# Performance work log

Measured on AMD Instinct MI355X. Metric: run time of the kernel, lower is better.

Reference implementation:

```python
import jax, jax.numpy as jnp
import numpy as np

HID = 2048
NEXP = 16
BRD = max(64, HID // 8)        # block_router_dim = 256
BATCH, SEQ = 4, 8192
BASE_BS, MAX_BS = 512, 2048
BASE_THR, BASE_BUDGET = 0.6, 0.3


def _adjust(seq_len):
    # mirrors _adjust_parameters_for_length (static: depends only on shape)
    if seq_len <= 4096:
        return BASE_BS, BASE_THR, BASE_BUDGET
    elif seq_len <= 16384:
        return min(1024, MAX_BS), BASE_THR * 1.1, BASE_BUDGET * 0.7
    else:
        scale = min(seq_len / 16384, 4)
        return min(int(BASE_BS * scale), MAX_BS), BASE_THR * 1.2, BASE_BUDGET * (1.0 / scale)


def _layernorm(x, g, b, eps=1e-5):
    m = x.mean(-1, keepdims=True)
    v = ((x - m) ** 2).mean(-1, keepdims=True)
    return (x - m) / jnp.sqrt(v + eps) * g + b


def setup_inputs() -> dict:
    key = jax.random.key(0)
    k = jax.random.split(key, 6)
    return {
        "hidden_states": jax.random.normal(k[0], (BATCH, SEQ, HID), jnp.float32),
        # block_router: Linear(H->256) -> LN -> GELU -> Linear(256->E)
        "bw1": jax.random.normal(k[1], (HID, BRD), jnp.float32) * 0.02,
        "bb1": jnp.zeros((BRD,), jnp.float32),
        "ln_g": jnp.ones((BRD,), jnp.float32),
        "ln_b": jnp.zeros((BRD,), jnp.float32),
        # final block-router layer scaled up so block entropies spread around the
        # 0.66 threshold and both routing branches are exercised
        "bw2": jax.random.normal(k[2], (BRD, NEXP), jnp.float32) * 0.6,
        "bb2": jnp.zeros((NEXP,), jnp.float32),
        # token_router: Linear(H->H/2) -> GELU -> (Dropout: eval/identity) -> Linear(H/2->E)
        "tw1": jax.random.normal(k[3], (HID, HID // 2), jnp.float32) * 0.02,
        "tb1": jnp.zeros((HID // 2,), jnp.float32),
        "tw2": jax.random.normal(k[4], (HID // 2, NEXP), jnp.float32) * 0.02,
        "tb2": jnp.zeros((NEXP,), jnp.float32),
    }


def reference(hidden_states, bw1, bb1, ln_g, ln_b, bw2, bb2, tw1, tb1, tw2, tb2):
    B, S, H = hidden_states.shape
    E = bw2.shape[1]
    bs, thr, budget = _adjust(S)
    assert S % bs == 0, "reference assumes seq_len divisible by block_size"
    N = S // bs
    max_tok = int(S * budget)               # python int (static)
    k_budget = max(1, max_tok // bs)        # blocks_within_budget (static)

    # --- block-level routing ---
    block_repr = hidden_states.reshape(B, N, bs, H).mean(2)          # [B,N,H]
    h = _layernorm(block_repr @ bw1 + bb1, ln_g, ln_b)
    block_logits = jax.nn.gelu(h, approximate=False) @ bw2 + bb2     # [B,N,E]
    block_probs = jax.nn.softmax(block_logits, -1)
    p = block_probs + 1e-10
    entropy = -jnp.sum(p * jnp.log(p), -1) / jnp.log(jnp.float32(E))  # [B,N]

    mask1 = entropy > thr
    total_high = mask1.sum()
    # budget-based threshold adjustment (k-th largest high entropy)
    flat_ent = jnp.where(mask1.ravel(), entropy.ravel(), -jnp.inf)
    kth = jnp.sort(flat_ent)[::-1][k_budget - 1]
    cond = (total_high * bs > max_tok) & (total_high > 0) & (k_budget < total_high)
    mask2 = jnp.where(cond, entropy > kth, mask1)

    # sequential token budget over flattened (batch, block) row-major order
    cum = jnp.cumsum(mask2.ravel().astype(jnp.int32) * bs).reshape(B, N)
    token_flag = mask2 & (cum <= max_tok)            # per-token routing
    block_flag = (~mask1) | (mask2 & ~token_flag)    # block-level routing

    # block weight scatter: argmax one-hot * max prob (detached, torch uses .item())
    bw = jax.lax.stop_gradient(
        jax.nn.one_hot(jnp.argmax(block_probs, -1), E, dtype=block_probs.dtype)
        * jnp.max(block_probs, -1, keepdims=True))   # [B,N,E]

    # token-level routing computed densely, masked (dropout in eval mode = identity)
    th = jax.nn.gelu(hidden_states @ tw1 + tb1, approximate=False)
    token_probs = jax.nn.softmax(th @ tw2 + tb2, -1)  # [B,S,E]

    tf = jnp.repeat(token_flag, bs, axis=1)[..., None]   # [B,S,1]
    bf = jnp.repeat(block_flag, bs, axis=1)[..., None]
    bw_tok = jnp.repeat(bw, bs, axis=1)                  # [B,S,E]
    routing = jnp.where(tf, token_probs, jnp.where(bf, bw_tok, jnp.zeros((), hidden_states.dtype)))

    usage = routing.mean((0, 1))
    target = 1.0 / E
    aux = jnp.sum(target * jnp.log(target / (usage + 1e-10)))
    return routing, aux
```

## Files before the change

kernel.cpp:

```cpp
#include <hip/hip_runtime.h>
#include <math.h>

#define BB 4
#define SS 8192
#define HH 2048
#define EE 16
#define BRD_ 256
#define BSZ 1024
#define NN 8
#define NB 32
#define MAXTOK 1720
#define HHALF 1024
#define TC 16
#define ROWS 64
#define KSP 32
#define KL 64
#define JL 64

__device__ inline void wave_flags(const double* __restrict__ ent, int l,
                                  int& flag_out, int& fb_out) {
  const double THR = 0.6 * 1.1;
  double e = (l < NB) ? ent[l] : -INFINITY;
  bool m1 = (l < NB) && (e > THR);
  unsigned long long m1mask = __ballot(m1);
  int th = __popcll(m1mask);
  double sel = m1 ? e : -INFINITY;
  #pragma unroll
  for (int o = 32; o; o >>= 1) sel = fmax(sel, __shfl_xor(sel, o));
  bool m2 = (th >= 2) ? ((l < NB) && (e > sel)) : m1;
  unsigned long long m2mask = __ballot(m2);
  int cum = __popcll(m2mask & ((2ULL << l) - 1ULL)) * BSZ;
  bool tf = m2 && (cum <= MAXTOK);
  bool bf = (l < NB) && ((!m1) || (m2 && !tf));
  flag_out = tf ? 1 : (bf ? 2 : 0);
  unsigned long long tfmask = __ballot(tf);
  fb_out = tfmask ? (__ffsll(tfmask) - 1) : -1;
}

__global__ __launch_bounds__(256) void k_bmean(const float* __restrict__ x,
                                               double* __restrict__ part) {
  int wg = blockIdx.x;
  int bn = wg >> 4, tc = wg & 15;
  int b = bn >> 3, n = bn & 7;
  int tid = threadIdx.x;
  const float* base = x + ((size_t)(b * SS + n * BSZ + tc * ROWS) * HH);
  double a0=0,a1=0,a2=0,a3=0,a4=0,a5=0,a6=0,a7=0;
  #pragma unroll 4
  for (int t = 0; t < ROWS; ++t) {
    const float4* r = (const float4*)(base + (size_t)t * HH);
    float4 u = r[tid];
    float4 v = r[tid + 256];
    a0 += u.x; a1 += u.y; a2 += u.z; a3 += u.w;
    a4 += v.x; a5 += v.y; a6 += v.z; a7 += v.w;
  }
  double* p = part + ((size_t)bn * TC + tc) * HH;
  int hA = tid * 4, hB = 1024 + tid * 4;
  p[hA] = a0; p[hA+1] = a1; p[hA+2] = a2; p[hA+3] = a3;
  p[hB] = a4; p[hB+1] = a5; p[hB+2] = a6; p[hB+3] = a7;
}

__global__ __launch_bounds__(256) void k_g1(const double* __restrict__ part,
    const float* __restrict__ bw1, double* __restrict__ g1part) {
  __shared__ double brs[NB][KL];
  __shared__ float  wsm[KL][JL];
  int bid = blockIdx.x;
  int kq = bid >> 2, jt = bid & 3;
  int k0 = kq * KL, j0 = jt * JL;
  int tid = threadIdx.x;
  #pragma unroll
  for (int i = 0; i < 8; ++i) {
    int e = i * 256 + tid;
    int bn = e >> 6, k = e & 63;
    const double* pp = part + ((size_t)bn * TC) * HH + k0 + k;
    double s = 0;
    #pragma unroll
    for (int tc = 0; tc < TC; ++tc) s += pp[(size_t)tc * HH];
    brs[bn][k] = s * (1.0 / BSZ);
  }
  #pragma unroll
  for (int i = 0; i < 4; ++i) {
    int f = i * 256 + tid;
    int r = f >> 4, c4 = f & 15;
    float4 v = *(const float4*)(bw1 + (size_t)(k0 + r) * BRD_ + j0 + c4 * 4);
    *(float4*)&wsm[r][c4 * 4] = v;
  }
  __syncthreads();
  int j = tid & 63;
  int bh = (tid >> 6) * 8;
  double acc[8];
  #pragma unroll
  for (int r = 0; r < 8; ++r) acc[r] = 0;
  #pragma unroll 8
  for (int k = 0; k < KL; ++k) {
    double wv = (double)wsm[k][j];
    #pragma unroll
    for (int r = 0; r < 8; ++r) acc[r] += brs[bh + r][k] * wv;
  }
  #pragma unroll
  for (int r = 0; r < 8; ++r)
    g1part[((size_t)kq * NB + bh + r) * BRD_ + j0 + j] = acc[r];
}

__global__ __launch_bounds__(256) void k_router2(const double* __restrict__ g1part,
    const float* __restrict__ bb1, const float* __restrict__ lng, const float* __restrict__ lnb,
    const float* __restrict__ bw2, const float* __restrict__ bb2,
    double* __restrict__ ent, float* __restrict__ bwv, int* __restrict__ bwi) {
  __shared__ double tg[BRD_];
  __shared__ double p3[16][EE];
  __shared__ double red[4];
  __shared__ double l2[EE];
  __shared__ double bcast;
  int bn = blockIdx.x, tid = threadIdx.x;

  double a = (double)bb1[tid];
  #pragma unroll
  for (int kq = 0; kq < KSP; ++kq) a += g1part[((size_t)kq * NB + bn) * BRD_ + tid];

  double v = a;
  for (int o = 32; o; o >>= 1) v += __shfl_down(v, o);
  if ((tid & 63) == 0) red[tid >> 6] = v;
  __syncthreads();
  if (tid == 0) bcast = (red[0] + red[1] + red[2] + red[3]) * (1.0 / BRD_);
  __syncthreads();
  double m = bcast;
  double d = a - m;
  v = d * d;
  for (int o = 32; o; o >>= 1) v += __shfl_down(v, o);
  if ((tid & 63) == 0) red[tid >> 6] = v;
  __syncthreads();
  if (tid == 0) bcast = (red[0] + red[1] + red[2] + red[3]) * (1.0 / BRD_);
  __syncthreads();
  double var = bcast;
  double xn = d / sqrt(var + 1e-5) * (double)lng[tid] + (double)lnb[tid];
  tg[tid] = 0.5 * xn * (1.0 + erf(xn * 0.7071067811865476));
  __syncthreads();

  {
    int e = tid & 15, jc = tid >> 4;
    double s = 0;
    const float* w2 = bw2 + (size_t)(jc * 16) * EE + e;
    #pragma unroll
    for (int jj = 0; jj < 16; ++jj) s += tg[jc * 16 + jj] * (double)w2[jj * EE];
    p3[jc][e] = s;
  }
  __syncthreads();
  if (tid < EE) {
    double acc = (double)bb2[tid];
    #pragma unroll
    for (int jc = 0; jc < 16; ++jc) acc += p3[jc][tid];
    l2[tid] = acc;
  }
  __syncthreads();

  if (tid < 64) {
    int e = tid & 15;
    double le = l2[e];
    double mx = le;
    #pragma unroll
    for (int o = 1; o < 16; o <<= 1) mx = fmax(mx, __shfl_xor(mx, o));
    double pe = exp(le - mx);
    double se = pe;
    #pragma unroll
    for (int o = 1; o < 16; o <<= 1) se += __shfl_xor(se, o);
    double pr = pe / se;
    double q = pr + 1e-10;
    double term = -q * log(q);
    double es = term;
    #pragma unroll
    for (int o = 1; o < 16; o <<= 1) es += __shfl_xor(es, o);
    double mp = pr;
    #pragma unroll
    for (int o = 1; o < 16; o <<= 1) mp = fmax(mp, __shfl_xor(mp, o));
    unsigned long long eqm = __ballot((tid < 16) && (pr == mp));
    if (tid == 0) {
      ent[bn] = es / log(16.0);
      bwv[bn] = (float)mp;
      bwi[bn] = __ffsll(eqm) - 1;
    }
  }
}

__global__ __launch_bounds__(256) void k_out(const double* __restrict__ ent,
    const float* __restrict__ bwv, const int* __restrict__ bwi,
    const float* __restrict__ x, const float* __restrict__ tw1, const float* __restrict__ tb1,
    const float* __restrict__ tw2, float* __restrict__ routing, float* __restrict__ lpart) {
  __shared__ int flg_s[NB + 1];
  __shared__ float xs[64][33];
  __shared__ float wsm[32][65];
  __shared__ float ths[64][65];
  int tid = threadIdx.x;
  int bid = blockIdx.x;
  if (tid < 64) {
    int f, fb;
    wave_flags(ent, tid, f, fb);
    if (tid < NB) flg_s[tid] = f;
    if (tid == 0) flg_s[NB] = fb;
  }
  __syncthreads();

  if (bid < 256) {
    int bn = bid >> 3, seg = bid & 7;
    int fl = flg_s[bn];
    if (fl == 1) return;
    int b = bn >> 3, n = bn & 7;
    float4 z = make_float4(0.f, 0.f, 0.f, 0.f);
    float4 val = z;
    int c_hit = -1;
    if (fl == 2) {
      int ai = bwi[bn];
      c_hit = ai >> 2;
      ((float*)&val)[ai & 3] = bwv[bn];
    }
    float4* out = (float4*)(routing + ((size_t)(b * SS + n * BSZ + seg * 128) * EE));
    #pragma unroll
    for (int l = 0; l < 2; ++l) {
      int idx = l * 256 + tid;
      int c = idx & 3;
      out[idx] = (c == c_hit) ? val : z;
    }
    return;
  }

  int fb = flg_s[NB];
  if (fb < 0) return;
  int b = fb >> 3, n = fb & 7;
  int tb = bid - 256;
  int tg = tb >> 4, nc = tb & 15;
  int t0 = tg * 64, j0 = nc * 64;
  const float* xb = x + ((size_t)(b * SS + n * BSZ + t0) * HH);
  int tr = tid >> 4, tc = tid & 15;
  float acc[4][4];
  for (int i = 0; i < 4; ++i)
    for (int j = 0; j < 4; ++j) acc[i][j] = tb1[j0 + tc + j * 16];
  for (int k0 = 0; k0 < HH; k0 += 32) {
    #pragma unroll
    for (int l = 0; l < 8; ++l) {
      int idx = l * 256 + tid; int r = idx >> 5, c = idx & 31;
      xs[r][c] = xb[(size_t)r * HH + k0 + c];
    }
    #pragma unroll
    for (int l = 0; l < 8; ++l) {
      int idx = l * 256 + tid; int r = idx >> 6, c = idx & 63;
      wsm[r][c] = tw1[(size_t)(k0 + r) * HHALF + j0 + c];
    }
    __syncthreads();
    #pragma unroll
    for (int kk = 0; kk < 32; ++kk) {
      float xv[4], wv[4];
      for (int i = 0; i < 4; ++i) xv[i] = xs[tr + i * 16][kk];
      for (int j = 0; j < 4; ++j) wv[j] = wsm[kk][tc + j * 16];
      for (int i = 0; i < 4; ++i)
        for (int j = 0; j < 4; ++j) acc[i][j] += xv[i] * wv[j];
    }
    __syncthreads();
  }
  for (int i = 0; i < 4; ++i)
    for (int j = 0; j < 4; ++j) {
      float aa = acc[i][j];
      ths[tr + i * 16][tc + j * 16] = 0.5f * aa * (1.0f + erff(aa * 0.70710678f));
    }
  __syncthreads();
  float* lp = lpart + (size_t)nc * (BSZ * EE);
  #pragma unroll
  for (int l = 0; l < 4; ++l) {
    int idx = l * 256 + tid; int t = idx >> 4, e = idx & 15;
    float s = 0;
    #pragma unroll
    for (int jj = 0; jj < 64; ++jj) s += ths[t][jj] * tw2[(size_t)(j0 + jj) * EE + e];
    lp[(t0 + t) * EE + e] = s;
  }
}

__global__ __launch_bounds__(64) void k_toksoft(const double* __restrict__ ent,
    const float* __restrict__ lpart, const float* __restrict__ tb2,
    float* __restrict__ routing, double* __restrict__ upart) {
  int tid = threadIdx.x;
  int f_unused, fb;
  wave_flags(ent, tid, f_unused, fb);
  if (fb < 0) return;
  int b = fb >> 3, n = fb & 7;
  int w = blockIdx.x;
  int t = w * 64 + tid;
  float l[EE];
  #pragma unroll
  for (int e = 0; e < EE; ++e) {
    float s = tb2[e];
    #pragma unroll
    for (int nc = 0; nc < 16; ++nc) s += lpart[(size_t)nc * (BSZ * EE) + t * EE + e];
    l[e] = s;
  }
  float mx = l[0];
  for (int e = 1; e < EE; ++e) mx = fmaxf(mx, l[e]);
  float se = 0;
  for (int e = 0; e < EE; ++e) { l[e] = expf(l[e] - mx); se += l[e]; }
  float inv = 1.0f / se;
  for (int e = 0; e < EE; ++e) l[e] *= inv;
  float4* orow = (float4*)(routing + ((size_t)(b * SS + n * BSZ + t) * EE));
  orow[0] = make_float4(l[0], l[1], l[2], l[3]);
  orow[1] = make_float4(l[4], l[5], l[6], l[7]);
  orow[2] = make_float4(l[8], l[9], l[10], l[11]);
  orow[3] = make_float4(l[12], l[13], l[14], l[15]);
  for (int e = 0; e < EE; ++e) {
    double v = (double)l[e];
    for (int o = 32; o; o >>= 1) v += __shfl_down(v, o);
    if (tid == 0) upart[w * EE + e] = v;
  }
}

__global__ __launch_bounds__(256) void k_aux(const double* __restrict__ ent,
    const double* __restrict__ upart, const float* __restrict__ bwv,
    const int* __restrict__ bwi, float* __restrict__ outaux) {
  __shared__ int flg_s[NB + 1];
  __shared__ double up[16][EE];
  __shared__ double blkc[NB];
  __shared__ int    blke[NB];
  __shared__ double us[EE];
  int tid = threadIdx.x;
  if (tid < 64) {
    int f, fb;
    wave_flags(ent, tid, f, fb);
    if (tid < NB) flg_s[tid] = f;
    if (tid == 0) flg_s[NB] = fb;
  }
  __syncthreads();
  int fb = flg_s[NB];
  if (fb >= 0) up[tid >> 4][tid & 15] = upart[tid];
  if (tid < NB) {
    int f = flg_s[tid];
    blkc[tid] = (f == 2) ? (double)BSZ * (double)bwv[tid] : 0.0;
    blke[tid] = (f == 2) ? bwi[tid] : -1;
  }
  __syncthreads();
  if (tid < EE) {
    double s = 0;
    if (fb >= 0) for (int w = 0; w < 16; ++w) s += up[w][tid];
    for (int i = 0; i < NB; ++i) if (blke[i] == tid) s += blkc[i];
    us[tid] = s;
  }
  __syncthreads();
  if (tid == 0) {
    double aux = 0;
    const double target = 1.0 / EE;
    for (int e = 0; e < EE; ++e) {
      double u = us[e] / (double)(BB * SS);
      aux += target * log(target / (u + 1e-10));
    }
    *outaux = (float)aux;
  }
}

extern "C" void kernel_launch(void* const* d_in, const int* in_sizes, int n_in,
                              void* d_out, int out_size, void* d_ws, size_t ws_size,
                              hipStream_t stream) {
  const float* x   = (const float*)d_in[0];
  const float* bw1 = (const float*)d_in[1];
  const float* bb1 = (const float*)d_in[2];
  const float* lng = (const float*)d_in[3];
  const float* lnb = (const float*)d_in[4];
  const float* bw2 = (const float*)d_in[5];
  const float* bb2 = (const float*)d_in[6];
  const float* tw1 = (const float*)d_in[7];
  const float* tb1 = (const float*)d_in[8];
  const float* tw2 = (const float*)d_in[9];
  const float* tb2 = (const float*)d_in[10];
  float* routing = (float*)d_out;
  float* outaux = routing + (size_t)BB * SS * EE;

  char* w = (char*)d_ws;
  size_t off = 0;
  double* part  = (double*)(w + off); off += (size_t)NB * TC * HH * 8;
  double* g1p   = (double*)(w + off); off += (size_t)KSP * NB * BRD_ * 8;
  float*  lpart = (float*) (w + off); off += 16 * (size_t)BSZ * EE * 4;
  double* upart = (double*)(w + off); off += 16 * EE * 8;
  double* ent   = (double*)(w + off); off += NB * 8;
  float*  bwv   = (float*) (w + off); off += 256;
  int*    bwi   = (int*)   (w + off); off += 256;

  hipLaunchKernelGGL(k_bmean,   dim3(NB * TC), dim3(256), 0, stream, x, part);
  hipLaunchKernelGGL(k_g1,      dim3(128),     dim3(256), 0, stream, part, bw1, g1p);
  hipLaunchKernelGGL(k_router2, dim3(NB),      dim3(256), 0, stream, g1p,
                     bb1, lng, lnb, bw2, bb2, ent, bwv, bwi);
  hipLaunchKernelGGL(k_out,     dim3(512),     dim3(256), 0, stream, ent, bwv, bwi,
                     x, tw1, tb1, tw2, routing, lpart);
  hipLaunchKernelGGL(k_toksoft, dim3(16),      dim3(64),  0, stream, ent, lpart, tb2,
                     routing, upart);
  hipLaunchKernelGGL(k_aux,     dim3(1),       dim3(256), 0, stream, ent, upart, bwv, bwi, outaux);
}
```

Baseline: 74.51 us.

## Use bf16 MFMA for token router GEMM and fuse softmax with aux kernel

Replaces the scalar FP32 outer-product loop in the token-router first layer with bf16 MFMA 16x16x32 instructions. Inputs and weights are converted to bf16 while staged into LDS, and the weight tile is stored transposed. The token softmax and aux-loss kernels are merged into one 1024-thread block, which removes a launch and the upart workspace round trip. Rounding to bf16 lowers the precision of the hidden activations, which may push outputs past tolerance.

```diff
diff --git a/kernel.cpp b/kernel.cpp
--- a/kernel.cpp
+++ b/kernel.cpp
@@ -17,6 +17,15 @@
 #define KL 64
 #define JL 64
 
+typedef __attribute__((ext_vector_type(8))) short bf16x8;
+typedef __attribute__((ext_vector_type(4))) float f32x4;
+
+__device__ inline short f2bf(float f) {
+  unsigned u = __builtin_bit_cast(unsigned, f);
+  u += 0x7FFFu + ((u >> 16) & 1u);
+  return (short)(u >> 16);
+}
+
 __device__ inline void wave_flags(const double* __restrict__ ent, int l,
                                   int& flag_out, int& fb_out) {
   const double THR = 0.6 * 1.1;
@@ -185,8 +194,8 @@
     const float* __restrict__ x, const float* __restrict__ tw1, const float* __restrict__ tb1,
     const float* __restrict__ tw2, float* __restrict__ routing, float* __restrict__ lpart) {
   __shared__ int flg_s[NB + 1];
-  __shared__ float xs[64][33];
-  __shared__ float wsm[32][65];
+  __shared__ short xs_bf[64][72];
+  __shared__ short wsT[64][72];
   __shared__ float ths[64][65];
   int tid = threadIdx.x;
   int bid = blockIdx.x;
@@ -228,37 +237,50 @@
   int tg = tb >> 4, nc = tb & 15;
   int t0 = tg * 64, j0 = nc * 64;
   const float* xb = x + ((size_t)(b * SS + n * BSZ + t0) * HH);
-  int tr = tid >> 4, tc = tid & 15;
-  float acc[4][4];
-  for (int i = 0; i < 4; ++i)
-    for (int j = 0; j < 4; ++j) acc[i][j] = tb1[j0 + tc + j * 16];
-  for (int k0 = 0; k0 < HH; k0 += 32) {
-    #pragma unroll
-    for (int l = 0; l < 8; ++l) {
-      int idx = l * 256 + tid; int r = idx >> 5, c = idx & 31;
-      xs[r][c] = xb[(size_t)r * HH + k0 + c];
-    }
-    #pragma unroll
-    for (int l = 0; l < 8; ++l) {
-      int idx = l * 256 + tid; int r = idx >> 6, c = idx & 63;
-      wsm[r][c] = tw1[(size_t)(k0 + r) * HHALF + j0 + c];
+  int wv = tid >> 6, lane = tid & 63;
+  int wm = (wv >> 1) * 32, wn = (wv & 1) * 32;
+  int fr = lane & 15, kg = lane >> 4;
+  f32x4 acc00 = {0,0,0,0}, acc01 = {0,0,0,0}, acc10 = {0,0,0,0}, acc11 = {0,0,0,0};
+
+  for (int k0 = 0; k0 < HH; k0 += 64) {
+    #pragma unroll
+    for (int i = 0; i < 16; ++i) {
+      int e = i * 256 + tid; int r = e >> 6, c = e & 63;
+      xs_bf[r][c] = f2bf(xb[(size_t)r * HH + k0 + c]);
+    }
+    #pragma unroll
+    for (int i = 0; i < 16; ++i) {
+      int e = i * 256 + tid; int r = e >> 6, c = e & 63;
+      wsT[c][r] = f2bf(tw1[(size_t)(k0 + r) * HHALF + j0 + c]);
     }
     __syncthreads();
     #pragma unroll
-    for (int kk = 0; kk < 32; ++kk) {
-      float xv[4], wv[4];
-      for (int i = 0; i < 4; ++i) xv[i] = xs[tr + i * 16][kk];
-      for (int j = 0; j < 4; ++j) wv[j] = wsm[kk][tc + j * 16];
-      for (int i = 0; i < 4; ++i)
-        for (int j = 0; j < 4; ++j) acc[i][j] += xv[i] * wv[j];
+    for (int kc = 0; kc < 64; kc += 32) {
+      int ks = kc + kg * 8;
+      bf16x8 a0 = *(const bf16x8*)&xs_bf[wm + fr][ks];
+      bf16x8 a1 = *(const bf16x8*)&xs_bf[wm + 16 + fr][ks];
+      bf16x8 b0 = *(const bf16x8*)&wsT[wn + fr][ks];
+      bf16x8 b1 = *(const bf16x8*)&wsT[wn + 16 + fr][ks];
+      acc00 = __builtin_amdgcn_mfma_f32_16x16x32_bf16(a0, b0, acc00, 0, 0, 0);
+      acc01 = __builtin_amdgcn_mfma_f32_16x16x32_bf16(a0, b1, acc01, 0, 0, 0);
+      acc10 = __builtin_amdgcn_mfma_f32_16x16x32_bf16(a1, b0, acc10, 0, 0, 0);
+      acc11 = __builtin_amdgcn_mfma_f32_16x16x32_bf16(a1, b1, acc11, 0, 0, 0);
     }
     __syncthreads();
   }
-  for (int i = 0; i < 4; ++i)
-    for (int j = 0; j < 4; ++j) {
-      float aa = acc[i][j];
-      ths[tr + i * 16][tc + j * 16] = 0.5f * aa * (1.0f + erff(aa * 0.70710678f));
-    }
+  #pragma unroll
+  for (int r = 0; r < 4; ++r) {
+    int row0 = wm + kg * 4 + r, row1 = wm + 16 + kg * 4 + r;
+    int col0 = wn + fr,         col1 = wn + 16 + fr;
+    float v00 = acc00[r] + tb1[j0 + col0];
+    float v01 = acc01[r] + tb1[j0 + col1];
+    float v10 = acc10[r] + tb1[j0 + col0];
+    float v11 = acc11[r] + tb1[j0 + col1];
+    ths[row0][col0] = 0.5f * v00 * (1.0f + erff(v00 * 0.70710678f));
+    ths[row0][col1] = 0.5f * v01 * (1.0f + erff(v01 * 0.70710678f));
+    ths[row1][col0] = 0.5f * v10 * (1.0f + erff(v10 * 0.70710678f));
+    ths[row1][col1] = 0.5f * v11 * (1.0f + erff(v11 * 0.70710678f));
+  }
   __syncthreads();
   float* lp = lpart + (size_t)nc * (BSZ * EE);
   #pragma unroll
@@ -271,49 +293,12 @@
   }
 }
 
-__global__ __launch_bounds__(64) void k_toksoft(const double* __restrict__ ent,
+__global__ __launch_bounds__(1024) void k_tail(const double* __restrict__ ent,
     const float* __restrict__ lpart, const float* __restrict__ tb2,
-    float* __restrict__ routing, double* __restrict__ upart) {
-  int tid = threadIdx.x;
-  int f_unused, fb;
-  wave_flags(ent, tid, f_unused, fb);
-  if (fb < 0) return;
-  int b = fb >> 3, n = fb & 7;
-  int w = blockIdx.x;
-  int t = w * 64 + tid;
-  float l[EE];
-  #pragma unroll
-  for (int e = 0; e < EE; ++e) {
-    float s = tb2[e];
-    #pragma unroll
-    for (int nc = 0; nc < 16; ++nc) s += lpart[(size_t)nc * (BSZ * EE) + t * EE + e];
-    l[e] = s;
-  }
-  float mx = l[0];
-  for (int e = 1; e < EE; ++e) mx = fmaxf(mx, l[e]);
-  float se = 0;
-  for (int e = 0; e < EE; ++e) { l[e] = expf(l[e] - mx); se += l[e]; }
-  float inv = 1.0f / se;
-  for (int e = 0; e < EE; ++e) l[e] *= inv;
-  float4* orow = (float4*)(routing + ((size_t)(b * SS + n * BSZ + t) * EE));
-  orow[0] = make_float4(l[0], l[1], l[2], l[3]);
-  orow[1] = make_float4(l[4], l[5], l[6], l[7]);
-  orow[2] = make_float4(l[8], l[9], l[10], l[11]);
-  orow[3] = make_float4(l[12], l[13], l[14], l[15]);
-  for (int e = 0; e < EE; ++e) {
-    double v = (double)l[e];
-    for (int o = 32; o; o >>= 1) v += __shfl_down(v, o);
-    if (tid == 0) upart[w * EE + e] = v;
-  }
-}
-
-__global__ __launch_bounds__(256) void k_aux(const double* __restrict__ ent,
-    const double* __restrict__ upart, const float* __restrict__ bwv,
-    const int* __restrict__ bwi, float* __restrict__ outaux) {
+    const float* __restrict__ bwv, const int* __restrict__ bwi,
+    float* __restrict__ routing, float* __restrict__ outaux) {
   __shared__ int flg_s[NB + 1];
   __shared__ double up[16][EE];
-  __shared__ double blkc[NB];
-  __shared__ int    blke[NB];
   __shared__ double us[EE];
   int tid = threadIdx.x;
   if (tid < 64) {
@@ -324,17 +309,41 @@
   }
   __syncthreads();
   int fb = flg_s[NB];
-  if (fb >= 0) up[tid >> 4][tid & 15] = upart[tid];
-  if (tid < NB) {
-    int f = flg_s[tid];
-    blkc[tid] = (f == 2) ? (double)BSZ * (double)bwv[tid] : 0.0;
-    blke[tid] = (f == 2) ? bwi[tid] : -1;
+  if (fb >= 0) {
+    int b = fb >> 3, n = fb & 7;
+    int t = tid;
+    float l[EE];
+    #pragma unroll
+    for (int e = 0; e < EE; ++e) {
+      float s = tb2[e];
+      #pragma unroll
+      for (int nc = 0; nc < 16; ++nc) s += lpart[(size_t)nc * (BSZ * EE) + t * EE + e];
+      l[e] = s;
+    }
+    float mx = l[0];
+    for (int e = 1; e < EE; ++e) mx = fmaxf(mx, l[e]);
+    float se = 0;
+    for (int e = 0; e < EE; ++e) { l[e] = expf(l[e] - mx); se += l[e]; }
+    float inv = 1.0f / se;
+    for (int e = 0; e < EE; ++e) l[e] *= inv;
+    float4* orow = (float4*)(routing + ((size_t)(b * SS + n * BSZ + t) * EE));
+    orow[0] = make_float4(l[0], l[1], l[2], l[3]);
+    orow[1] = make_float4(l[4], l[5], l[6], l[7]);
+    orow[2] = make_float4(l[8], l[9], l[10], l[11]);
+    orow[3] = make_float4(l[12], l[13], l[14], l[15]);
+    int w = tid >> 6;
+    for (int e = 0; e < EE; ++e) {
+      double v = (double)l[e];
+      for (int o = 32; o; o >>= 1) v += __shfl_down(v, o);
+      if ((tid & 63) == 0) up[w][e] = v;
+    }
   }
   __syncthreads();
   if (tid < EE) {
     double s = 0;
     if (fb >= 0) for (int w = 0; w < 16; ++w) s += up[w][tid];
-    for (int i = 0; i < NB; ++i) if (blke[i] == tid) s += blkc[i];
+    for (int i = 0; i < NB; ++i)
+      if (flg_s[i] == 2 && bwi[i] == tid) s += (double)BSZ * (double)bwv[i];
     us[tid] = s;
   }
   __syncthreads();
@@ -371,18 +380,16 @@
   double* part  = (double*)(w + off); off += (size_t)NB * TC * HH * 8;
   double* g1p   = (double*)(w + off); off += (size_t)KSP * NB * BRD_ * 8;
   float*  lpart = (float*) (w + off); off += 16 * (size_t)BSZ * EE * 4;
-  double* upart = (double*)(w + off); off += 16 * EE * 8;
   double* ent   = (double*)(w + off); off += NB * 8;
   float*  bwv   = (float*) (w + off); off += 256;
   int*    bwi   = (int*)   (w + off); off += 256;
 
-  hipLaunchKernelGGL(k_bmean,   dim3(NB * TC), dim3(256), 0, stream, x, part);
-  hipLaunchKernelGGL(k_g1,      dim3(128),     dim3(256), 0, stream, part, bw1, g1p);
-  hipLaunchKernelGGL(k_router2, dim3(NB),      dim3(256), 0, stream, g1p,
+  hipLaunchKernelGGL(k_bmean,   dim3(NB * TC), dim3(256),  0, stream, x, part);
+  hipLaunchKernelGGL(k_g1,      dim3(128),     dim3(256),  0, stream, part, bw1, g1p);
+  hipLaunchKernelGGL(k_router2, dim3(NB),      dim3(256),  0, stream, g1p,
                      bb1, lng, lnb, bw2, bb2, ent, bwv, bwi);
-  hipLaunchKernelGGL(k_out,     dim3(512),     dim3(256), 0, stream, ent, bwv, bwi,
+  hipLaunchKernelGGL(k_out,     dim3(512),     dim3(256),  0, stream, ent, bwv, bwi,
                      x, tw1, tb1, tw2, routing, lpart);
-  hipLaunchKernelGGL(k_toksoft, dim3(16),      dim3(64),  0, stream, ent, lpart, tb2,
-                     routing, upart);
-  hipLaunchKernelGGL(k_aux,     dim3(1),       dim3(256), 0, stream, ent, upart, bwv, bwi, outaux);
-}
+  hipLaunchKernelGGL(k_tail,    dim3(1),       dim3(1024), 0, stream, ent, lpart, tb2,
+                     bwv, bwi, routing, outaux);
+}
```

New measurement: 75.12 us. About the same (+0.8%).
